# Performance work log

Measured on AMD Instinct MI355X. Metric: run time of the kernel, lower is better.

The kernel has to match this reference:

```python
import jax, jax.numpy as jnp
import numpy as np

N_NODES = 50000


def _gcn_conv(x, row, col, W, b, n_nodes):
    # symmetric-norm GCN conv with self loops already appended to (row, col)
    deg = jax.ops.segment_sum(jnp.ones_like(row, dtype=x.dtype), row, num_segments=n_nodes)
    # every node has a self loop, so deg >= 1; pow(-0.5) is finite
    dis = deg ** -0.5
    norm = dis[row] * dis[col]                       # [E']
    msg = x[row] * norm[:, None]                     # gather + scale  [E', d]
    agg = jax.ops.segment_sum(msg, col, num_segments=n_nodes)  # scatter-add [N, d]
    return agg @ W + b


def setup_inputs() -> dict:
    key = jax.random.key(0)
    ks = jax.random.split(key, 12)
    N, E, Q, d_in, h = N_NODES, 800000, 200000, 64, 128
    x = jax.random.normal(ks[0], (N, d_in), dtype=jnp.float32)
    edge_index = jax.random.randint(ks[1], (2, E), 0, N)
    edge_label_index = jax.random.randint(ks[2], (2, Q), 0, N)
    def lin(k, fan_in, fan_out):
        kw, kb = jax.random.split(k)
        bound = 1.0 / np.sqrt(fan_in)
        W = jax.random.uniform(kw, (fan_in, fan_out), minval=-bound, maxval=bound, dtype=jnp.float32)
        b = jax.random.uniform(kb, (fan_out,), minval=-bound, maxval=bound, dtype=jnp.float32)
        return W, b
    W1, b1 = lin(ks[3], d_in, h)
    W2, b2 = lin(ks[4], h, h)
    Wc1, bc1 = lin(ks[5], 2 * h, h)
    Wc2, bc2 = lin(ks[6], h, 1)
    return {"x": x, "edge_index": edge_index, "edge_label_index": edge_label_index,
            "W1": W1, "b1": b1, "W2": W2, "b2": b2,
            "Wc1": Wc1, "bc1": bc1, "Wc2": Wc2, "bc2": bc2}


def reference(x, edge_index, edge_label_index, W1, b1, W2, b2, Wc1, bc1, Wc2, bc2):
    n = x.shape[0]
    loops = jnp.arange(n, dtype=edge_index.dtype)
    row = jnp.concatenate([edge_index[0], loops])
    col = jnp.concatenate([edge_index[1], loops])
    h1 = jax.nn.relu(_gcn_conv(x, row, col, W1, b1, n))
    h2 = _gcn_conv(h1, row, col, W2, b2, n)
    src, dst = edge_label_index[0], edge_label_index[1]
    h = jnp.concatenate([h2[src], h2[dst]], axis=1)  # [Q, 2*hidden]
    h = jax.nn.relu(h @ Wc1 + bc1)
    return h @ Wc2 + bc2                              # [Q, 1]
```

## Files before the change

### kernel.cpp

```cpp
#include <hip/hip_runtime.h>


#define HB 128
#define NWIN 16384

typedef __attribute__((ext_vector_type(8))) short short8;
typedef __attribute__((ext_vector_type(4))) float floatx4;

static __device__ __forceinline__ unsigned int f2bf(float v) {
    union { float f; unsigned int u; } c; c.f = v;
    unsigned int lsb = (c.u >> 16) & 1u;
    c.u += 0x7FFFu + lsb;
    return c.u >> 16;
}
static __device__ __forceinline__ float bf2f(unsigned int h) {
    union { float f; unsigned int u; } c; c.u = h << 16;
    return c.f;
}

__global__ __launch_bounds__(256) void k_pre(const int* __restrict__ row,
                                             const int* __restrict__ col,
                                             unsigned int* __restrict__ hRow,
                                             unsigned int* __restrict__ hCol,
                                             const float* __restrict__ x,
                                             unsigned int* __restrict__ xb,
                                             const float* __restrict__ W1,
                                             const float* __restrict__ W2,
                                             const float* __restrict__ Wc1,
                                             const float* __restrict__ b2,
                                             const float* __restrict__ bc1,
                                             unsigned short* __restrict__ UVhi,
                                             unsigned short* __restrict__ UVlo,
                                             unsigned short* __restrict__ W1hi,
                                             unsigned short* __restrict__ W1lo,
                                             float* __restrict__ buv,
                                             int E, int N, int W, int chunk,
                                             int nHist, int nXb) {
    __shared__ unsigned int lds[NWIN];
    int t = threadIdx.x, b = blockIdx.x;
    if (b < nHist) {
        int hb = b % HB;
        int yb = b / HB;
        int p = yb >> 1, win = yb & 1;
        int base = win * NWIN;
        int wcap = min(W - base, NWIN);
        if (wcap <= 0) return;
        const int* idxArr = p ? col : row;
        unsigned int* outArr = p ? hCol : hRow;
        int e0 = hb * chunk, e1 = min(E, e0 + chunk);
        for (int i = t; i < wcap; i += 256) lds[i] = 0;
        __syncthreads();
        for (int e = e0 + t; e < e1; e += 256) {
            int idx = idxArr[e];
            int w = (idx >> 1) - base;
            if ((unsigned)w < (unsigned)wcap)
                atomicAdd(&lds[w], 1u << ((idx & 1) * 16));
        }
        __syncthreads();
        for (int i = t; i < wcap; i += 256)
            outArr[(size_t)hb * W + base + i] = lds[i];
    } else if (b < nHist + nXb) {
        int i = (b - nHist) * 256 + t;
        if (i < N * 32) {
            float2 v = ((const float2*)x)[i];
            xb[i] = f2bf(v.x) | (f2bf(v.y) << 16);
        }
    } else {
        int bf = b - nHist - nXb;
        float* w2row = (float*)lds;
        if (bf < 128) {
            int k = bf;
            int j = t & 127, half = t >> 7;
            int n = half * 128 + j;
            const float* wc = Wc1 + (size_t)half * 128 * 128 + j;
            if (t < 128) w2row[t] = W2[k * 128 + t];
            __syncthreads();
            float acc = 0.f;
#pragma unroll 8
            for (int m = 0; m < 128; m++) acc += w2row[m] * wc[(size_t)m * 128];
            int kstep = k >> 5, kl = k & 31, quad = kl >> 3, j8 = kl & 7;
            int nb = n >> 4, l = quad * 16 + (n & 15);
            int pidx = ((kstep * 16 + nb) * 64 + l) * 8 + j8;
            unsigned int h = f2bf(acc);
            UVhi[pidx] = (unsigned short)h;
            UVlo[pidx] = (unsigned short)f2bf(acc - bf2f(h));
        } else if (bf == 128) {
            int j = t & 127, half = t >> 7;
            const float* wc = Wc1 + (size_t)half * 128 * 128 + j;
            float acc = half ? 0.f : bc1[j];
#pragma unroll 8
            for (int m = 0; m < 128; m++) acc += b2[m] * wc[(size_t)m * 128];
            buv[half * 128 + j] = acc;
        } else {
            int idx = (bf - 129) * 256 + t;
            int k = idx >> 7, n = idx & 127;
            float v = W1[k * 128 + n];
            int kstep = k >> 5, kl = k & 31, quad = kl >> 3, j8 = kl & 7;
            int nb = n >> 4, l = quad * 16 + (n & 15);
            int pidx = ((kstep * 8 + nb) * 64 + l) * 8 + j8;
            unsigned int h = f2bf(v);
            W1hi[pidx] = (unsigned short)h;
            W1lo[pidx] = (unsigned short)f2bf(v - bf2f(h));
        }
    }
}

__global__ __launch_bounds__(256) void k_reduce(const unsigned int* __restrict__ hRow,
                                                unsigned int* __restrict__ hCol,
                                                int* __restrict__ cntCol,
                                                float* __restrict__ dis,
                                                int N, int W) {
    int w = blockIdx.x * 256 + threadIdx.x;
    if (w >= W) return;
    unsigned int r0 = 0, r1 = 0, c0 = 0, c1 = 0;
#pragma unroll 8
    for (int b = 0; b < HB; b++) {
        size_t idx = (size_t)b * W + w;
        unsigned int hr = hRow[idx];
        unsigned int hc = hCol[idx];
        hCol[idx] = c0 | (c1 << 16);
        r0 += hr & 0xFFFFu; r1 += hr >> 16;
        c0 += hc & 0xFFFFu; c1 += hc >> 16;
    }
    int n0 = 2 * w, n1 = 2 * w + 1;
    cntCol[n0] = (int)c0;
    dis[n0] = 1.0f / sqrtf((float)(r0 + 1));
    if (n1 < N) {
        cntCol[n1] = (int)c1;
        dis[n1] = 1.0f / sqrtf((float)(r1 + 1));
    }
}

__global__ __launch_bounds__(256) void k_scan1(const int* __restrict__ cnt,
                                               int* __restrict__ offs,
                                               int* __restrict__ bsum, int N) {
    __shared__ int ts[256];
    int t = threadIdx.x;
    int base = blockIdx.x * 1024 + t * 4;
    int v0 = (base + 0 < N) ? cnt[base + 0] : 0;
    int v1 = (base + 1 < N) ? cnt[base + 1] : 0;
    int v2 = (base + 2 < N) ? cnt[base + 2] : 0;
    int v3 = (base + 3 < N) ? cnt[base + 3] : 0;
    int sum = v0 + v1 + v2 + v3;
    ts[t] = sum;
    __syncthreads();
    for (int off = 1; off < 256; off <<= 1) {
        int x = (t >= off) ? ts[t - off] : 0;
        __syncthreads();
        ts[t] += x;
        __syncthreads();
    }
    int e = ts[t] - sum;
    if (base + 0 < N) offs[base + 0] = e;
    if (base + 1 < N) offs[base + 1] = e + v0;
    if (base + 2 < N) offs[base + 2] = e + v0 + v1;
    if (base + 3 < N) offs[base + 3] = e + v0 + v1 + v2;
    if (t == 255) bsum[blockIdx.x] = ts[255];
}

__global__ __launch_bounds__(256) void k_scan2(int* __restrict__ bsum, int B) {
    __shared__ int ts[256];
    int t = threadIdx.x;
    int v = (t < B) ? bsum[t] : 0;
    ts[t] = v;
    __syncthreads();
    for (int off = 1; off < 256; off <<= 1) {
        int x = (t >= off) ? ts[t - off] : 0;
        __syncthreads();
        ts[t] += x;
        __syncthreads();
    }
    if (t < B) bsum[t] = ts[t] - v;
}

__global__ __launch_bounds__(256) void k_scan3(int* __restrict__ offs,
                                               const int* __restrict__ bsum,
                                               int N, int E) {
    int i = blockIdx.x * 256 + threadIdx.x;
    if (i < N) offs[i] = offs[i] + bsum[i >> 10];
    if (i == 0) offs[N] = E;
}

__global__ __launch_bounds__(256) void k_fill3(const int* __restrict__ row,
                                               const int* __restrict__ col,
                                               const int* __restrict__ offs,
                                               const unsigned int* __restrict__ hCol,
                                               int* __restrict__ srcSorted,
                                               int E, int N, int W, int chunk) {
    __shared__ int base[NWIN];
    int t = threadIdx.x, b = blockIdx.x;
    int n0 = blockIdx.y * NWIN;
    int nCnt = min(NWIN, N - n0);
    int e0 = b * chunk, e1 = min(E, e0 + chunk);
    for (int wl = t; wl * 2 < nCnt; wl += 256) {
        unsigned int pref = hCol[(size_t)b * W + (n0 >> 1) + wl];
        int nn = n0 + wl * 2;
        base[wl * 2] = offs[nn] + (int)(pref & 0xFFFFu);
        if (wl * 2 + 1 < nCnt)
            base[wl * 2 + 1] = offs[nn + 1] + (int)(pref >> 16);
    }
    __syncthreads();
    for (int e = e0 + t; e < e1; e += 256) {
        int c = col[e] - n0;
        if ((unsigned)c < (unsigned)nCnt) {
            int pos = atomicAdd(&base[c], 1);
            srcSorted[pos] = row[e];
        }
    }
}

__global__ __launch_bounds__(256) void k_conv1(const unsigned short* __restrict__ s,
                                               const int* __restrict__ offs,
                                               const int* __restrict__ srcs,
                                               const float* __restrict__ dis,
                                               const unsigned short* __restrict__ Bhi,
                                               const unsigned short* __restrict__ Blo,
                                               const float* __restrict__ b1,
                                               unsigned short* __restrict__ h1b, int N) {
    __shared__ unsigned short Ahi[16][72];
    __shared__ unsigned short Alo[16][72];
    int t = threadIdx.x;
    int lane = t & 63, wave = t >> 6;
    int quad = lane >> 4;
    short8 bh[2][2], bl[2][2];
#pragma unroll
    for (int ks = 0; ks < 2; ks++)
#pragma unroll
        for (int nt = 0; nt < 2; nt++) {
            int nb = wave * 2 + nt;
            bh[ks][nt] = *(const short8*)(Bhi + ((ks * 8 + nb) * 64 + lane) * 8);
            bl[ks][nt] = *(const short8*)(Blo + ((ks * 8 + nb) * 64 + lane) * 8);
        }
    {
        int nl = t >> 4;
        int node = blockIdx.x * 16 + nl;
        if (node < N) {
            int c4 = (t & 15) * 4;
            int e = offs[node], eEnd = offs[node + 1];
            float dn = dis[node];
            uint2 w = *(const uint2*)(s + (size_t)node * 64 + c4);
            float4 acc;
            acc.x = bf2f(w.x & 0xFFFF) * dn; acc.y = bf2f(w.x >> 16) * dn;
            acc.z = bf2f(w.y & 0xFFFF) * dn; acc.w = bf2f(w.y >> 16) * dn;
            while (e + 1 < eEnd) {
                int sA = srcs[e], sB = srcs[e + 1];
                float dA = dis[sA], dB = dis[sB];
                uint2 vA = *(const uint2*)(s + (size_t)sA * 64 + c4);
                uint2 vB = *(const uint2*)(s + (size_t)sB * 64 + c4);
                acc.x += bf2f(vA.x & 0xFFFF) * dA + bf2f(vB.x & 0xFFFF) * dB;
                acc.y += bf2f(vA.x >> 16) * dA + bf2f(vB.x >> 16) * dB;
                acc.z += bf2f(vA.y & 0xFFFF) * dA + bf2f(vB.y & 0xFFFF) * dB;
                acc.w += bf2f(vA.y >> 16) * dA + bf2f(vB.y >> 16) * dB;
                e += 2;
            }
            if (e < eEnd) {
                int sA = srcs[e];
                float dA = dis[sA];
                uint2 vA = *(const uint2*)(s + (size_t)sA * 64 + c4);
                acc.x += bf2f(vA.x & 0xFFFF) * dA; acc.y += bf2f(vA.x >> 16) * dA;
                acc.z += bf2f(vA.y & 0xFFFF) * dA; acc.w += bf2f(vA.y >> 16) * dA;
            }
            acc.x *= dn; acc.y *= dn; acc.z *= dn; acc.w *= dn;
            unsigned int h0 = f2bf(acc.x), h1 = f2bf(acc.y),
                         h2 = f2bf(acc.z), h3 = f2bf(acc.w);
            uint2 hw; hw.x = h0 | (h1 << 16); hw.y = h2 | (h3 << 16);
            uint2 lw;
            lw.x = f2bf(acc.x - bf2f(h0)) | (f2bf(acc.y - bf2f(h1)) << 16);
            lw.y = f2bf(acc.z - bf2f(h2)) | (f2bf(acc.w - bf2f(h3)) << 16);
            *(uint2*)(&Ahi[nl][c4]) = hw;
            *(uint2*)(&Alo[nl][c4]) = lw;
        }
    }
    __syncthreads();
    int ml = lane & 15;
    floatx4 acc[2] = {};
#pragma unroll
    for (int ks = 0; ks < 2; ks++) {
        short8 ahi = *(const short8*)(&Ahi[ml][ks * 32 + quad * 8]);
        short8 alo = *(const short8*)(&Alo[ml][ks * 32 + quad * 8]);
#pragma unroll
        for (int nt = 0; nt < 2; nt++) {
            acc[nt] = __builtin_amdgcn_mfma_f32_16x16x32_bf16(ahi, bh[ks][nt], acc[nt], 0, 0, 0);
            acc[nt] = __builtin_amdgcn_mfma_f32_16x16x32_bf16(ahi, bl[ks][nt], acc[nt], 0, 0, 0);
            acc[nt] = __builtin_amdgcn_mfma_f32_16x16x32_bf16(alo, bh[ks][nt], acc[nt], 0, 0, 0);
        }
    }
    int md = blockIdx.x * 16 + quad * 4;
#pragma unroll
    for (int nt = 0; nt < 2; nt++) {
        int n0 = (wave * 2 + nt) * 16 + (lane & 15);
        float bias = b1[n0];
#pragma unroll
        for (int r = 0; r < 4; r++) {
            int node = md + r;
            if (node < N)
                h1b[(size_t)node * 128 + n0] =
                    (unsigned short)f2bf(fmaxf(acc[nt][r] + bias, 0.f) * dis[node]);
        }
    }
}

__global__ __launch_bounds__(256) void k_gather2(const unsigned short* __restrict__ s,
                                                 const int* __restrict__ offs,
                                                 const int* __restrict__ srcs,
                                                 const float* __restrict__ dis,
                                                 unsigned short* __restrict__ agg,
                                                 int N) {
    int tid = blockIdx.x * 256 + threadIdx.x;
    int node = tid >> 4;
    if (node >= N) return;
    int c8 = (tid & 15) * 8;
    int e = offs[node], eEnd = offs[node + 1];
    float dn = dis[node];
    uint4 w = *(const uint4*)(s + (size_t)node * 128 + c8);
    float a0 = bf2f(w.x & 0xFFFF), a1 = bf2f(w.x >> 16);
    float a2 = bf2f(w.y & 0xFFFF), a3 = bf2f(w.y >> 16);
    float a4 = bf2f(w.z & 0xFFFF), a5 = bf2f(w.z >> 16);
    float a6 = bf2f(w.w & 0xFFFF), a7 = bf2f(w.w >> 16);
    while (e + 1 < eEnd) {
        int sA = srcs[e], sB = srcs[e + 1];
        uint4 vA = *(const uint4*)(s + (size_t)sA * 128 + c8);
        uint4 vB = *(const uint4*)(s + (size_t)sB * 128 + c8);
        a0 += bf2f(vA.x & 0xFFFF) + bf2f(vB.x & 0xFFFF);
        a1 += bf2f(vA.x >> 16) + bf2f(vB.x >> 16);
        a2 += bf2f(vA.y & 0xFFFF) + bf2f(vB.y & 0xFFFF);
        a3 += bf2f(vA.y >> 16) + bf2f(vB.y >> 16);
        a4 += bf2f(vA.z & 0xFFFF) + bf2f(vB.z & 0xFFFF);
        a5 += bf2f(vA.z >> 16) + bf2f(vB.z >> 16);
        a6 += bf2f(vA.w & 0xFFFF) + bf2f(vB.w & 0xFFFF);
        a7 += bf2f(vA.w >> 16) + bf2f(vB.w >> 16);
        e += 2;
    }
    if (e < eEnd) {
        int sA = srcs[e];
        uint4 vA = *(const uint4*)(s + (size_t)sA * 128 + c8);
        a0 += bf2f(vA.x & 0xFFFF); a1 += bf2f(vA.x >> 16);
        a2 += bf2f(vA.y & 0xFFFF); a3 += bf2f(vA.y >> 16);
        a4 += bf2f(vA.z & 0xFFFF); a5 += bf2f(vA.z >> 16);
        a6 += bf2f(vA.w & 0xFFFF); a7 += bf2f(vA.w >> 16);
    }
    uint4 o;
    o.x = f2bf(a0 * dn) | (f2bf(a1 * dn) << 16);
    o.y = f2bf(a2 * dn) | (f2bf(a3 * dn) << 16);
    o.z = f2bf(a4 * dn) | (f2bf(a5 * dn) << 16);
    o.w = f2bf(a6 * dn) | (f2bf(a7 * dn) << 16);
    *(uint4*)(agg + (size_t)node * 128 + c8) = o;
}

__global__ __launch_bounds__(256) void k_mfmaUV(const unsigned short* __restrict__ A,
                                                const unsigned short* __restrict__ Bhi,
                                                const unsigned short* __restrict__ Blo,
                                                const float* __restrict__ buv,
                                                unsigned short* __restrict__ Ub,
                                                unsigned short* __restrict__ Vb, int N) {
    int lane = threadIdx.x & 63, wave = threadIdx.x >> 6;
    int quad = lane >> 4;
    short8 bh[4][4], bl[4][4];
#pragma unroll
    for (int ks = 0; ks < 4; ks++)
#pragma unroll
        for (int nt = 0; nt < 4; nt++) {
            int nb = wave * 4 + nt;
            bh[ks][nt] = *(const short8*)(Bhi + ((ks * 16 + nb) * 64 + lane) * 8);
            bl[ks][nt] = *(const short8*)(Blo + ((ks * 16 + nb) * 64 + lane) * 8);
        }
#pragma unroll
    for (int g = 0; g < 4; g++) {
        int mbase = blockIdx.x * 64 + g * 16;
        int ma = mbase + (lane & 15); if (ma >= N) ma = N - 1;
        floatx4 acc[4] = {};
#pragma unroll
        for (int ks = 0; ks < 4; ks++) {
            short8 a = *(const short8*)(A + (size_t)ma * 128 + ks * 32 + quad * 8);
#pragma unroll
            for (int nt = 0; nt < 4; nt++) {
                acc[nt] = __builtin_amdgcn_mfma_f32_16x16x32_bf16(a, bh[ks][nt], acc[nt], 0, 0, 0);
                acc[nt] = __builtin_amdgcn_mfma_f32_16x16x32_bf16(a, bl[ks][nt], acc[nt], 0, 0, 0);
            }
        }
        int md = mbase + quad * 4;
#pragma unroll
        for (int nt = 0; nt < 4; nt++) {
            int n0 = wave * 64 + nt * 16 + (lane & 15);
            float bias = buv[n0];
            unsigned short* dst = (n0 < 128) ? Ub : Vb;
            int cc = n0 & 127;
#pragma unroll
            for (int r = 0; r < 4; r++) {
                int node = md + r;
                if (node < N)
                    dst[(size_t)node * 128 + cc] =
                        (unsigned short)f2bf(acc[nt][r] + bias);
            }
        }
    }
}

__global__ __launch_bounds__(256) void k_head(const unsigned short* __restrict__ Ub,
                                              const unsigned short* __restrict__ Vb,
                                              const int* __restrict__ srcA,
                                              const int* __restrict__ dstA,
                                              const float* __restrict__ Wc2,
                                              const float* __restrict__ bc2,
                                              float* __restrict__ out, int Q) {
    int t = threadIdx.x;
    int q = blockIdx.x * 16 + (t >> 4);
    if (q >= Q) return;
    int l = t & 15;
    int s = srcA[q], d = dstA[q];
    uint4 u = *(const uint4*)(Ub + (size_t)s * 128 + l * 8);
    uint4 v = *(const uint4*)(Vb + (size_t)d * 128 + l * 8);
    const float4* w = (const float4*)(Wc2 + l * 8);
    float4 w0 = w[0], w1 = w[1];
    float acc = 0.f, z;
    z = fmaxf(bf2f(u.x & 0xFFFF) + bf2f(v.x & 0xFFFF), 0.f); acc += z * w0.x;
    z = fmaxf(bf2f(u.x >> 16)    + bf2f(v.x >> 16),    0.f); acc += z * w0.y;
    z = fmaxf(bf2f(u.y & 0xFFFF) + bf2f(v.y & 0xFFFF), 0.f); acc += z * w0.z;
    z = fmaxf(bf2f(u.y >> 16)    + bf2f(v.y >> 16),    0.f); acc += z * w0.w;
    z = fmaxf(bf2f(u.z & 0xFFFF) + bf2f(v.z & 0xFFFF), 0.f); acc += z * w1.x;
    z = fmaxf(bf2f(u.z >> 16)    + bf2f(v.z >> 16),    0.f); acc += z * w1.y;
    z = fmaxf(bf2f(u.w & 0xFFFF) + bf2f(v.w & 0xFFFF), 0.f); acc += z * w1.z;
    z = fmaxf(bf2f(u.w >> 16)    + bf2f(v.w >> 16),    0.f); acc += z * w1.w;
    acc += __shfl_xor(acc, 1);
    acc += __shfl_xor(acc, 2);
    acc += __shfl_xor(acc, 4);
    acc += __shfl_xor(acc, 8);
    if (l == 0) out[q] = acc + bc2[0];
}

extern "C" void kernel_launch(void* const* d_in, const int* in_sizes, int n_in,
                              void* d_out, int out_size, void* d_ws, size_t ws_size,
                              hipStream_t stream) {
    const float* x   = (const float*)d_in[0];
    const int*   ei  = (const int*)d_in[1];
    const int*   eli = (const int*)d_in[2];
    const float* W1  = (const float*)d_in[3];
    const float* b1  = (const float*)d_in[4];
    const float* W2  = (const float*)d_in[5];
    const float* b2  = (const float*)d_in[6];
    const float* Wc1 = (const float*)d_in[7];
    const float* bc1 = (const float*)d_in[8];
    const float* Wc2 = (const float*)d_in[9];
    const float* bc2 = (const float*)d_in[10];
    float* out = (float*)d_out;
    char* wsb = (char*)d_ws;

    const int N = in_sizes[0] / 64;
    const int E = in_sizes[1] / 2;
    const int Q = in_sizes[2] / 2;
    const int W = (N + 1) / 2;
    const int chunk = (E + HB - 1) / HB;
    const int nPass = (N + NWIN - 1) / NWIN;
    const int nWinH = (W + NWIN - 1) / NWIN;
    const int nHist = HB * 2 * nWinH;
    const int nXb   = (N * 32 + 255) / 256;

    float* dis       = (float*)wsb;
    int*   offs      = (int*)wsb + 65536;
    int*   bsum      = (int*)wsb + 197120;
    int*   cntCol    = (int*)wsb + 197376;
    float* buv       = (float*)wsb + 262912;
    unsigned short* UVhi = (unsigned short*)((int*)wsb + 263168);
    unsigned short* UVlo = (unsigned short*)((int*)wsb + 279552);
    unsigned short* W1hi = (unsigned short*)((int*)wsb + 295936);
    unsigned short* W1lo = (unsigned short*)((int*)wsb + 300032);
    int*   srcSorted = (int*)wsb + 304128;
    unsigned short* Vb   = (unsigned short*)((int*)wsb + 1104128);
    unsigned short* h1b  = (unsigned short*)((int*)wsb + 4304128);
    unsigned short* agg2b= (unsigned short*)((int*)wsb + 7504128);
    unsigned short* Ub = h1b;
    unsigned int* hRow = (unsigned int*)wsb + 10704128;
    unsigned int* hCol = (unsigned int*)wsb + 13904128;
    unsigned int* xb   = (unsigned int*)wsb + 17104128;

    const int* row  = ei;
    const int* col  = ei + E;
    const int* srcA = eli;
    const int* dstA = eli + Q;

    const int scanB = (N + 1023) / 1024;

    k_pre<<<nHist + nXb + 161, 256, 0, stream>>>(
        row, col, hRow, hCol, x, xb, W1, W2, Wc1, b2, bc1,
        UVhi, UVlo, W1hi, W1lo, buv, E, N, W, chunk, nHist, nXb);
    k_reduce<<<(W + 255) / 256, 256, 0, stream>>>(hRow, hCol, cntCol, dis, N, W);
    k_scan1<<<scanB, 256, 0, stream>>>(cntCol, offs, bsum, N);
    k_scan2<<<1, 256, 0, stream>>>(bsum, scanB);
    k_scan3<<<(N + 255) / 256, 256, 0, stream>>>(offs, bsum, N, E);
    k_fill3<<<dim3(HB, nPass), 256, 0, stream>>>(row, col, offs, hCol, srcSorted, E, N, W, chunk);
    k_conv1<<<(N + 15) / 16, 256, 0, stream>>>(
        (const unsigned short*)xb, offs, srcSorted, dis, W1hi, W1lo, b1, h1b, N);
    k_gather2<<<((size_t)N * 16 + 255) / 256, 256, 0, stream>>>(
        h1b, offs, srcSorted, dis, agg2b, N);
    k_mfmaUV<<<(N + 63) / 64, 256, 0, stream>>>(agg2b, UVhi, UVlo, buv, Ub, Vb, N);
    k_head<<<(Q + 15) / 16, 256, 0, stream>>>(Ub, Vb, srcA, dstA, Wc2, bc2, out, Q);
}
```

Baseline: 261.5 us.

## Fuse histogram reduce with block scan and halve histogram block count

Merges the per-node histogram reduction kernel with the first-level prefix scan, so column counts are scanned in registers and shared memory and the cntCol buffer disappears. Each block now covers 512 nodes instead of 1024, and scan3 indexes block sums accordingly. Separately, the number of histogram partitions HB drops from 128 to 64. That halves the histogram memory and the reduce loop length, but each partition handles twice as many edges in k_pre and k_fill3, so those kernels have less parallelism.

```diff
diff --git a/kernel.cpp b/kernel.cpp
--- a/kernel.cpp
+++ b/kernel.cpp
@@ -1,7 +1,7 @@
 #include <hip/hip_runtime.h>
 
 
-#define HB 128
+#define HB 64
 #define NWIN 16384
 
 typedef __attribute__((ext_vector_type(8))) short short8;
@@ -105,56 +105,45 @@
     }
 }
 
-__global__ __launch_bounds__(256) void k_reduce(const unsigned int* __restrict__ hRow,
-                                                unsigned int* __restrict__ hCol,
-                                                int* __restrict__ cntCol,
-                                                float* __restrict__ dis,
-                                                int N, int W) {
-    int w = blockIdx.x * 256 + threadIdx.x;
-    if (w >= W) return;
-    unsigned int r0 = 0, r1 = 0, c0 = 0, c1 = 0;
-#pragma unroll 8
-    for (int b = 0; b < HB; b++) {
-        size_t idx = (size_t)b * W + w;
-        unsigned int hr = hRow[idx];
-        unsigned int hc = hCol[idx];
-        hCol[idx] = c0 | (c1 << 16);
-        r0 += hr & 0xFFFFu; r1 += hr >> 16;
-        c0 += hc & 0xFFFFu; c1 += hc >> 16;
-    }
-    int n0 = 2 * w, n1 = 2 * w + 1;
-    cntCol[n0] = (int)c0;
-    dis[n0] = 1.0f / sqrtf((float)(r0 + 1));
-    if (n1 < N) {
-        cntCol[n1] = (int)c1;
-        dis[n1] = 1.0f / sqrtf((float)(r1 + 1));
-    }
-}
-
-__global__ __launch_bounds__(256) void k_scan1(const int* __restrict__ cnt,
-                                               int* __restrict__ offs,
-                                               int* __restrict__ bsum, int N) {
+__global__ __launch_bounds__(256) void k_rs(const unsigned int* __restrict__ hRow,
+                                            unsigned int* __restrict__ hCol,
+                                            float* __restrict__ dis,
+                                            int* __restrict__ offs,
+                                            int* __restrict__ bsum,
+                                            int N, int W) {
     __shared__ int ts[256];
     int t = threadIdx.x;
-    int base = blockIdx.x * 1024 + t * 4;
-    int v0 = (base + 0 < N) ? cnt[base + 0] : 0;
-    int v1 = (base + 1 < N) ? cnt[base + 1] : 0;
-    int v2 = (base + 2 < N) ? cnt[base + 2] : 0;
-    int v3 = (base + 3 < N) ? cnt[base + 3] : 0;
-    int sum = v0 + v1 + v2 + v3;
+    int w = blockIdx.x * 256 + t;
+    unsigned int r0 = 0, r1 = 0, c0 = 0, c1 = 0;
+    if (w < W) {
+#pragma unroll 8
+        for (int b = 0; b < HB; b++) {
+            size_t idx = (size_t)b * W + w;
+            unsigned int hr = hRow[idx];
+            unsigned int hc = hCol[idx];
+            hCol[idx] = c0 | (c1 << 16);
+            r0 += hr & 0xFFFFu; r1 += hr >> 16;
+            c0 += hc & 0xFFFFu; c1 += hc >> 16;
+        }
+        int n0 = 2 * w, n1 = 2 * w + 1;
+        dis[n0] = 1.0f / sqrtf((float)(r0 + 1));
+        if (n1 < N) dis[n1] = 1.0f / sqrtf((float)(r1 + 1));
+    }
+    int sum = (w < W) ? (int)(c0 + c1) : 0;
     ts[t] = sum;
     __syncthreads();
     for (int off = 1; off < 256; off <<= 1) {
-        int x = (t >= off) ? ts[t - off] : 0;
-        __syncthreads();
-        ts[t] += x;
+        int xv = (t >= off) ? ts[t - off] : 0;
+        __syncthreads();
+        ts[t] += xv;
         __syncthreads();
     }
     int e = ts[t] - sum;
-    if (base + 0 < N) offs[base + 0] = e;
-    if (base + 1 < N) offs[base + 1] = e + v0;
-    if (base + 2 < N) offs[base + 2] = e + v0 + v1;
-    if (base + 3 < N) offs[base + 3] = e + v0 + v1 + v2;
+    if (w < W) {
+        int n0 = 2 * w, n1 = 2 * w + 1;
+        offs[n0] = e;
+        if (n1 < N) offs[n1] = e + (int)c0;
+    }
     if (t == 255) bsum[blockIdx.x] = ts[255];
 }
 
@@ -177,7 +166,7 @@
                                                const int* __restrict__ bsum,
                                                int N, int E) {
     int i = blockIdx.x * 256 + threadIdx.x;
-    if (i < N) offs[i] = offs[i] + bsum[i >> 10];
+    if (i < N) offs[i] = offs[i] + bsum[i >> 9];
     if (i == 0) offs[N] = E;
 }
 
@@ -454,11 +443,11 @@
     const int nWinH = (W + NWIN - 1) / NWIN;
     const int nHist = HB * 2 * nWinH;
     const int nXb   = (N * 32 + 255) / 256;
+    const int rsB   = (W + 255) / 256;
 
     float* dis       = (float*)wsb;
     int*   offs      = (int*)wsb + 65536;
     int*   bsum      = (int*)wsb + 197120;
-    int*   cntCol    = (int*)wsb + 197376;
     float* buv       = (float*)wsb + 262912;
     unsigned short* UVhi = (unsigned short*)((int*)wsb + 263168);
     unsigned short* UVlo = (unsigned short*)((int*)wsb + 279552);
@@ -470,22 +459,19 @@
     unsigned short* agg2b= (unsigned short*)((int*)wsb + 7504128);
     unsigned short* Ub = h1b;
     unsigned int* hRow = (unsigned int*)wsb + 10704128;
-    unsigned int* hCol = (unsigned int*)wsb + 13904128;
-    unsigned int* xb   = (unsigned int*)wsb + 17104128;
+    unsigned int* hCol = (unsigned int*)wsb + 12304128;
+    unsigned int* xb   = (unsigned int*)wsb + 13904128;
 
     const int* row  = ei;
     const int* col  = ei + E;
     const int* srcA = eli;
     const int* dstA = eli + Q;
 
-    const int scanB = (N + 1023) / 1024;
-
     k_pre<<<nHist + nXb + 161, 256, 0, stream>>>(
         row, col, hRow, hCol, x, xb, W1, W2, Wc1, b2, bc1,
         UVhi, UVlo, W1hi, W1lo, buv, E, N, W, chunk, nHist, nXb);
-    k_reduce<<<(W + 255) / 256, 256, 0, stream>>>(hRow, hCol, cntCol, dis, N, W);
-    k_scan1<<<scanB, 256, 0, stream>>>(cntCol, offs, bsum, N);
-    k_scan2<<<1, 256, 0, stream>>>(bsum, scanB);
+    k_rs<<<rsB, 256, 0, stream>>>(hRow, hCol, dis, offs, bsum, N, W);
+    k_scan2<<<1, 256, 0, stream>>>(bsum, rsB);
     k_scan3<<<(N + 255) / 256, 256, 0, stream>>>(offs, bsum, N, E);
     k_fill3<<<dim3(HB, nPass), 256, 0, stream>>>(row, col, offs, hCol, srcSorted, E, N, W, chunk);
     k_conv1<<<(N + 15) / 16, 256, 0, stream>>>(
```

New measurement: 258.0 us. Within noise of the previous version (-1.3%).
